# Optimization experiments

Measured on AMD Instinct MI355X. Metric: run time of the kernel, lower is better.

The kernel has to match this reference:

```python
import jax, jax.numpy as jnp
import numpy as np
import math

B, T, HID, H = 2, 2048, 2048, 16
D = HID // H  # 128
START_RATIO, RECENT_RATIO = 0.1, 0.25
ROPE_THETA = 10000.0


def setup_inputs() -> dict:
    key = jax.random.key(0)
    k1, k2, k3, k4, k5 = jax.random.split(key, 5)
    hidden_states = jax.random.normal(k1, (B, T, HID), jnp.float32)
    causal = jnp.tril(jnp.ones((T, T), bool))
    attention_mask = jnp.broadcast_to(
        jnp.where(causal, 0.0, jnp.finfo(jnp.float32).min)[None, None], (B, 1, T, T)
    )
    q_w = 0.02 * jax.random.normal(k2, (HID, HID), jnp.float32)
    k_w = 0.02 * jax.random.normal(k3, (HID, HID), jnp.float32)
    v_w = 0.02 * jax.random.normal(k4, (HID, HID), jnp.float32)
    o_w = 0.02 * jax.random.normal(k5, (HID, HID), jnp.float32)
    return dict(hidden_states=hidden_states, attention_mask=attention_mask,
                q_w=q_w, k_w=k_w, v_w=v_w, o_w=o_w)


def _rotate_half(x):
    x1, x2 = x[..., : D // 2], x[..., D // 2:]
    return jnp.concatenate([-x2, x1], axis=-1)


def _local_cam_mask(V, A_bar, recent_budget):
    # V: [B,H,K,D], A_bar: [B,H,K]
    K = V.shape[-2]
    m = recent_budget
    if m <= 0 or m >= K:
        return V
    evict_idx = max(0, min(K - m - 1, K - 1))
    ws = max(0, K - m)
    avg_window = jnp.clip(jnp.mean(A_bar[..., ws:], axis=-1), 1e-6, None)  # [B,H]
    prob = jnp.clip(A_bar[..., evict_idx] / avg_window, 0.0, 1.0)
    prob = jnp.nan_to_num(prob, nan=0.0, posinf=1.0, neginf=0.0)
    mask = jax.lax.stop_gradient(
        jax.random.bernoulli(jax.random.key(42), prob).astype(V.dtype)
    )  # [B,H]
    v_e = V[..., evict_idx, :] * mask[..., None] / m  # [B,H,D]
    return V.at[..., ws:, :].add(v_e[..., None, :])


def reference(hidden_states, attention_mask, q_w, k_w, v_w, o_w):
    MIN = jnp.finfo(hidden_states.dtype).min
    hs = jnp.nan_to_num(hidden_states, nan=0.0, posinf=1e4, neginf=-1e4)

    def proj(w):
        return (hs @ w.T).reshape(B, T, H, D).transpose(0, 2, 1, 3)  # [B,H,T,D]

    Q, K, V = proj(q_w), proj(k_w), proj(v_w)

    # rotary embedding (standard Llama)
    pos = jnp.arange(T, dtype=jnp.float32)
    inv_freq = 1.0 / (ROPE_THETA ** (jnp.arange(0, D, 2, dtype=jnp.float32) / D))
    freqs = pos[:, None] * inv_freq[None, :]  # [T, D/2]
    emb = jnp.concatenate([freqs, freqs], axis=-1)  # [T, D]
    cos, sin = jnp.cos(emb)[None, None], jnp.sin(emb)[None, None]
    Q = Q * cos + _rotate_half(Q) * sin
    K = K * cos + _rotate_half(K) * sin

    scores = jnp.einsum('bhtd,bhkd->bhtk', Q, K) / math.sqrt(D) + attention_mask
    scores = jnp.nan_to_num(scores, nan=MIN, posinf=MIN, neginf=MIN)
    attn = jax.nn.softmax(scores, axis=-1)  # [B,H,T,T]

    # first call: A_bar = detached last-row attention
    A_bar = jax.lax.stop_gradient(attn[..., -1, :])  # [B,H,T]

    k_len = T
    sb = max(0, min(int(START_RATIO * k_len), k_len))
    rb = max(0, min(int(RECENT_RATIO * k_len), k_len - sb))
    V = _local_cam_mask(V, A_bar, rb)

    attn_out = jnp.einsum('bhtk,bhkd->bhtd', attn, V)
    out = attn_out.transpose(0, 2, 1, 3).reshape(B, T, HID)
    return out @ o_w.T
```

## Files before the change

kernel.cpp:

```cpp
#include <hip/hip_runtime.h>
#include <cstdint>
#include <cstddef>


#define DEVINL __device__ __forceinline__

typedef float  f32x4  __attribute__((ext_vector_type(4)));
typedef __bf16 bf16x8 __attribute__((ext_vector_type(8)));

DEVINL float bf2f(unsigned short u){
  unsigned int x = ((unsigned int)u) << 16;
  return __builtin_bit_cast(float, x);
}
DEVINL void store_bf(unsigned short* p, float f){
  *(__bf16*)p = (__bf16)f;
}

DEVINL void load_lds16(const void* g, void* l){
  __builtin_amdgcn_global_load_lds(
      (const __attribute__((address_space(1))) void*)g,
      (__attribute__((address_space(3))) void*)l, 16, 0, 0);
}

#define QSCALE 0.127517432f

__global__ void cvt_all_kernel(const float* __restrict__ hs, const float* __restrict__ qw,
                               const float* __restrict__ kw, const float* __restrict__ vw,
                               const float* __restrict__ ow,
                               unsigned short* __restrict__ hsb, unsigned short* __restrict__ qwb,
                               unsigned short* __restrict__ kwb, unsigned short* __restrict__ vwb,
                               unsigned short* __restrict__ owb){
  int i = blockIdx.x * 256 + threadIdx.x;
  const float* s; unsigned short* d; int off;
  if (i < 2097152){ s = hs; d = hsb; off = i; }
  else {
    int j = i - 2097152; int w = j >> 20; off = j & 1048575;
    s = (w == 0) ? qw : (w == 1) ? kw : (w == 2) ? vw : ow;
    d = (w == 0) ? qwb : (w == 1) ? kwb : (w == 2) ? vwb : owb;
  }
  float4 v = reinterpret_cast<const float4*>(s)[off];
  unsigned short o[4];
  store_bf(&o[0], v.x); store_bf(&o[1], v.y); store_bf(&o[2], v.z); store_bf(&o[3], v.w);
  reinterpret_cast<uint2*>(d)[off] = *reinterpret_cast<uint2*>(o);
}

template<int MODE>
__global__ __launch_bounds__(256, 3)
void gemm_bt_kernel(const unsigned short* __restrict__ A,
                    const unsigned short* __restrict__ B,
                    unsigned short* __restrict__ Qo, unsigned short* __restrict__ Ko,
                    unsigned short* __restrict__ Vo, float* __restrict__ Co,
                    int M, int N, int K){
  __shared__ unsigned short As[128 * 64];
  __shared__ unsigned short Bs[128 * 64];
  const int tid = threadIdx.x, wave = tid >> 6, lane = tid & 63;
  const int m16 = lane & 15, quad = lane >> 4;
  const int m0 = blockIdx.y * 128, n0 = blockIdx.x * 128;
  const int wm = wave >> 1, wn = wave & 1;

  f32x4 acc[4][4] = {};

  for (int k0 = 0; k0 < K; k0 += 64){
    __syncthreads();
    #pragma unroll
    for (int i = 0; i < 4; ++i){
      int r  = wave * 32 + i * 8 + (lane >> 3);
      int c8 = (lane & 7) ^ (r & 7);
      load_lds16(A + (size_t)(m0 + r) * K + k0 + c8 * 8, &As[(wave * 32 + i * 8) * 64]);
      load_lds16(B + (size_t)(n0 + r) * K + k0 + c8 * 8, &Bs[(wave * 32 + i * 8) * 64]);
    }
    __syncthreads();
    #pragma unroll
    for (int kc = 0; kc < 2; ++kc){
      bf16x8 af[4], bfr[4];
      #pragma unroll
      for (int mt = 0; mt < 4; ++mt){
        int r = wm * 64 + mt * 16 + m16;
        af[mt] = *reinterpret_cast<const bf16x8*>(&As[(r * 8 + ((quad + 4 * kc) ^ (r & 7))) * 8]);
      }
      #pragma unroll
      for (int nt = 0; nt < 4; ++nt){
        int r = wn * 64 + nt * 16 + m16;
        bfr[nt] = *reinterpret_cast<const bf16x8*>(&Bs[(r * 8 + ((quad + 4 * kc) ^ (r & 7))) * 8]);
      }
      #pragma unroll
      for (int mt = 0; mt < 4; ++mt)
        #pragma unroll
        for (int nt = 0; nt < 4; ++nt)
          acc[mt][nt] = __builtin_amdgcn_mfma_f32_16x16x32_bf16(af[mt], bfr[nt], acc[mt][nt], 0, 0, 0);
    }
  }

  #pragma unroll
  for (int mt = 0; mt < 4; ++mt){
    #pragma unroll
    for (int nt = 0; nt < 4; ++nt){
      #pragma unroll
      for (int reg = 0; reg < 4; ++reg){
        int m = m0 + wm * 64 + mt * 16 + quad * 4 + reg;
        int n = n0 + wn * 64 + nt * 16 + m16;
        float v = acc[mt][nt][reg];
        if constexpr (MODE == 0){
          int which = n >> 11;
          int nn = n & 2047;
          int bq = m >> 11, t = m & 2047, hd = nn >> 7, dd = nn & 127;
          if (which == 0)
            store_bf(&Qo[((((size_t)bq) * 16 + hd) * 2048 + t) * 128 + dd], v);
          else if (which == 1)
            store_bf(&Ko[((((size_t)bq) * 16 + hd) * 2048 + t) * 128 + dd], v);
          else
            store_bf(&Vo[((((size_t)bq) * 16 + hd) * 128 + dd) * 2048 + t], v);
        } else {
          Co[(size_t)m * N + n] = v;
        }
      }
    }
  }
}

__global__ void rope_kernel(unsigned short* __restrict__ Q, unsigned short* __restrict__ K){
  int gid = blockIdx.x * 256 + threadIdx.x;
  int d2 = gid & 63;
  int t  = (gid >> 6) & 2047;
  int bh = (gid >> 17) & 31;
  int isK = gid >> 22;
  unsigned short* P = isK ? K : Q;
  float sc = isK ? 1.0f : QSCALE;
  size_t base = ((size_t)bh * 2048 + t) * 128;
  float x1 = bf2f(P[base + d2]);
  float x2 = bf2f(P[base + d2 + 64]);
  float inv = expf(-(float)d2 * 0.14391156606007266f);
  float fr = (float)t * inv;
  float sn, cs;
  sincosf(fr, &sn, &cs);
  store_bf(&P[base + d2],      (x1 * cs - x2 * sn) * sc);
  store_bf(&P[base + d2 + 64], (x2 * cs + x1 * sn) * sc);
}

DEVINL unsigned int rotl32(unsigned int x, int r){ return (x << r) | (x >> (32 - r)); }

__device__ float threefry_u01(int i){
  unsigned int c0 = (i < 16) ? (unsigned)i : (unsigned)(i - 16);
  unsigned int c1 = (i < 16) ? (unsigned)(i + 16) : (unsigned)i;
  bool hi = (i >= 16);
  unsigned int k0 = 0u, k1 = 42u, k2 = 0x1BD11BDAu ^ k0 ^ k1;
  unsigned int ks[3] = {k0, k1, k2};
  unsigned int x0 = c0 + k0, x1 = c1 + k1;
  const int R0[4] = {13, 15, 26, 6}, R1[4] = {17, 29, 16, 24};
  #pragma unroll
  for (int r = 0; r < 5; ++r){
    const int* RR = (r & 1) ? R1 : R0;
    #pragma unroll
    for (int j = 0; j < 4; ++j){ x0 += x1; x1 = rotl32(x1, RR[j]); x1 ^= x0; }
    x0 += ks[(r + 1) % 3];
    x1 += ks[(r + 2) % 3] + (unsigned)(r + 1);
  }
  unsigned int bits = hi ? x1 : x0;
  return __builtin_bit_cast(float, (bits >> 9) | 0x3f800000u) - 1.0f;
}

DEVINL float wred_max(float v){
  #pragma unroll
  for (int m = 1; m < 64; m <<= 1) v = fmaxf(v, __shfl_xor(v, m));
  return v;
}
DEVINL float wred_sum(float v){
  #pragma unroll
  for (int m = 1; m < 64; m <<= 1) v += __shfl_xor(v, m);
  return v;
}

__global__ __launch_bounds__(256)
void cam_kernel(const unsigned short* __restrict__ Q,
                const unsigned short* __restrict__ K,
                unsigned short* __restrict__ Vt){
  const int bh = blockIdx.x, tid = threadIdx.x;
  __shared__ float qv[128];
  __shared__ float redm[4], reds[4], redw[4];
  __shared__ float e1535s;
  __shared__ float bc0;
  if (tid < 128) qv[tid] = bf2f(Q[((size_t)bh * 2048 + 2047) * 128 + tid]);
  __syncthreads();

  float sc[8];
  float smax = -1e30f;
  #pragma unroll
  for (int j = 0; j < 8; ++j){
    int k = tid + j * 256;
    const uint4* kr4 = reinterpret_cast<const uint4*>(K + ((size_t)bh * 2048 + k) * 128);
    float acc = 0.f;
    #pragma unroll
    for (int c = 0; c < 16; ++c){
      uint4 pk = kr4[c];
      acc += qv[c * 8 + 0] * bf2f((unsigned short)(pk.x & 0xffff));
      acc += qv[c * 8 + 1] * bf2f((unsigned short)(pk.x >> 16));
      acc += qv[c * 8 + 2] * bf2f((unsigned short)(pk.y & 0xffff));
      acc += qv[c * 8 + 3] * bf2f((unsigned short)(pk.y >> 16));
      acc += qv[c * 8 + 4] * bf2f((unsigned short)(pk.z & 0xffff));
      acc += qv[c * 8 + 5] * bf2f((unsigned short)(pk.z >> 16));
      acc += qv[c * 8 + 6] * bf2f((unsigned short)(pk.w & 0xffff));
      acc += qv[c * 8 + 7] * bf2f((unsigned short)(pk.w >> 16));
    }
    sc[j] = acc;
    smax = fmaxf(smax, sc[j]);
  }
  int wave = tid >> 6, lane = tid & 63;
  float wm = wred_max(smax);
  if (lane == 0) redm[wave] = wm;
  __syncthreads();
  float M = fmaxf(fmaxf(redm[0], redm[1]), fmaxf(redm[2], redm[3]));
  float tsum = 0.f, wsum = 0.f;
  #pragma unroll
  for (int j = 0; j < 8; ++j){
    int k = tid + j * 256;
    float e = exp2f(sc[j] - M);
    if (k == 1535) e1535s = e;
    tsum += e;
    if (k >= 1536) wsum += e;
  }
  tsum = wred_sum(tsum); wsum = wred_sum(wsum);
  if (lane == 0){ reds[wave] = tsum; redw[wave] = wsum; }
  __syncthreads();
  if (tid == 0){
    float sum = reds[0] + reds[1] + reds[2] + reds[3];
    float wsm = redw[0] + redw[1] + redw[2] + redw[3];
    float abar = e1535s / sum;
    float avg  = fmaxf(wsm / (512.f * sum), 1e-6f);
    float pr   = abar / avg;
    pr = fminf(fmaxf(pr, 0.f), 1.f);
    float u = threefry_u01(bh);
    bc0 = (u < pr) ? (1.f / 512.f) : 0.f;
  }
  __syncthreads();
  float ves = bc0;
  if (ves != 0.f){
    for (int idx = tid; idx < 128 * 64; idx += 256){
      int d = idx >> 6, c = idx & 63;
      unsigned short* row = Vt + ((size_t)bh * 128 + d) * 2048;
      float ve = bf2f(row[1535]) * ves;
      uint4* p = reinterpret_cast<uint4*>(row + 1536) + c;
      uint4 pk = *p;
      unsigned short h[8];
      store_bf(&h[0], bf2f((unsigned short)(pk.x & 0xffff)) + ve);
      store_bf(&h[1], bf2f((unsigned short)(pk.x >> 16)) + ve);
      store_bf(&h[2], bf2f((unsigned short)(pk.y & 0xffff)) + ve);
      store_bf(&h[3], bf2f((unsigned short)(pk.y >> 16)) + ve);
      store_bf(&h[4], bf2f((unsigned short)(pk.z & 0xffff)) + ve);
      store_bf(&h[5], bf2f((unsigned short)(pk.z >> 16)) + ve);
      store_bf(&h[6], bf2f((unsigned short)(pk.w & 0xffff)) + ve);
      store_bf(&h[7], bf2f((unsigned short)(pk.w >> 16)) + ve);
      pk.x = (unsigned)h[0] | ((unsigned)h[1] << 16);
      pk.y = (unsigned)h[2] | ((unsigned)h[3] << 16);
      pk.z = (unsigned)h[4] | ((unsigned)h[5] << 16);
      pk.w = (unsigned)h[6] | ((unsigned)h[7] << 16);
      *p = pk;
    }
  }
}

__global__ __launch_bounds__(256, 2)
void flash_kernel(const unsigned short* __restrict__ Q,
                  const unsigned short* __restrict__ K,
                  const unsigned short* __restrict__ Vt,
                  unsigned short* __restrict__ AO){
  __shared__ unsigned short Qs[64 * 128];
  __shared__ unsigned short Ks[2][64 * 128];
  __shared__ unsigned short Vs[2][128 * 64];
  const int g = blockIdx.x, bh = blockIdx.y;
  const int tid = threadIdx.x, wave = tid >> 6, lane = tid & 63;
  const int m16 = lane & 15, quad = lane >> 4;
  unsigned short* Pw = Qs + wave * 2048;
  const int b = bh >> 4, h = bh & 15;

  bf16x8 onesf;
  #pragma unroll
  for (int j = 0; j < 8; ++j) onesf[j] = (__bf16)1.0f;

  #pragma unroll 1
  for (int phase = 0; phase < 2; ++phase){
    const int qt = phase ? (31 - g) : g;
    const int nk = qt + 1;

    {
      size_t qb = ((size_t)bh * 2048 + (size_t)qt * 64) * 128;
      #pragma unroll
      for (int i = 0; i < 4; ++i){
        int r   = wave * 16 + i * 4 + (lane >> 4);
        int c16 = (lane & 15) ^ (r & 15);
        load_lds16(Q + qb + (size_t)r * 128 + c16 * 8, &Qs[(wave * 16 + i * 4) * 128]);
      }
    }
    __syncthreads();
    bf16x8 qf[4];
    {
      int r = wave * 16 + m16;
      #pragma unroll
      for (int kc = 0; kc < 4; ++kc)
        qf[kc] = *reinterpret_cast<const bf16x8*>(&Qs[(r * 16 + ((quad + 4 * kc) ^ (r & 15))) * 8]);
    }

    f32x4 oacc[8] = {};
    f32x4 oaccL = {};
    f32x4 mst = {-1e30f, -1e30f, -1e30f, -1e30f};

    auto stageKV = [&](int kt, int buf){
      size_t kb = ((size_t)bh * 2048 + (size_t)kt * 64) * 128;
      #pragma unroll
      for (int i = 0; i < 4; ++i){
        int r   = wave * 16 + i * 4 + (lane >> 4);
        int c16 = (lane & 15) ^ (r & 15);
        load_lds16(K + kb + (size_t)r * 128 + c16 * 8, &Ks[buf][(wave * 16 + i * 4) * 128]);
      }
      size_t vb = (size_t)bh * 128 * 2048 + (size_t)kt * 64;
      #pragma unroll
      for (int i = 0; i < 4; ++i){
        int r  = wave * 32 + i * 8 + (lane >> 3);
        int c8 = (lane & 7) ^ (r & 7);
        load_lds16(Vt + vb + (size_t)r * 2048 + c8 * 8, &Vs[buf][(wave * 32 + i * 8) * 64]);
      }
    };

    stageKV(0, 0);
    #pragma unroll 1
    for (int t = 0; t < nk; ++t){
      const int buf = t & 1;
      __syncthreads();
      if (t + 1 < nk) stageKV(t + 1, buf ^ 1);

      f32x4 s[4] = {};
      #pragma unroll
      for (int kc = 0; kc < 4; ++kc){
        #pragma unroll
        for (int nt = 0; nt < 4; ++nt){
          int r = nt * 16 + m16;
          bf16x8 kf = *reinterpret_cast<const bf16x8*>(&Ks[buf][(r * 16 + ((quad + 4 * kc) ^ (r & 15))) * 8]);
          s[nt] = __builtin_amdgcn_mfma_f32_16x16x32_bf16(qf[kc], kf, s[nt], 0, 0, 0);
        }
      }
      if (t == nk - 1){
        int lrow = wave * 16 + quad * 4;
        #pragma unroll
        for (int nt = 0; nt < 4; ++nt)
          #pragma unroll
          for (int reg = 0; reg < 4; ++reg)
            if (nt * 16 + m16 > lrow + reg) s[nt][reg] = -1e30f;
      }
      f32x4 av;
      #pragma unroll
      for (int reg = 0; reg < 4; ++reg){
        float rm = fmaxf(fmaxf(s[0][reg], s[1][reg]), fmaxf(s[2][reg], s[3][reg]));
        rm = fmaxf(rm, __shfl_xor(rm, 1));
        rm = fmaxf(rm, __shfl_xor(rm, 2));
        rm = fmaxf(rm, __shfl_xor(rm, 4));
        rm = fmaxf(rm, __shfl_xor(rm, 8));
        float mold = mst[reg];
        float mnew = fmaxf(mold, rm);
        av[reg] = exp2f(mold - mnew);
        mst[reg] = mnew;
        #pragma unroll
        for (int nt = 0; nt < 4; ++nt)
          s[nt][reg] = exp2f(s[nt][reg] - mnew);
      }
      oaccL *= av;
      #pragma unroll
      for (int dt = 0; dt < 8; ++dt) oacc[dt] *= av;

      #pragma unroll
      for (int nt = 0; nt < 4; ++nt)
        #pragma unroll
        for (int reg = 0; reg < 4; ++reg){
          int r   = quad * 4 + reg;
          int col = nt * 16 + m16;
          store_bf(&Pw[(r * 8 + ((col >> 3) ^ (r & 7))) * 8 + (col & 7)], s[nt][reg]);
        }
      #pragma unroll
      for (int kc = 0; kc < 2; ++kc){
        bf16x8 pf = *reinterpret_cast<const bf16x8*>(&Pw[(m16 * 8 + ((quad + 4 * kc) ^ (m16 & 7))) * 8]);
        oaccL = __builtin_amdgcn_mfma_f32_16x16x32_bf16(pf, onesf, oaccL, 0, 0, 0);
        #pragma unroll
        for (int dt = 0; dt < 8; ++dt){
          int r = dt * 16 + m16;
          bf16x8 vf = *reinterpret_cast<const bf16x8*>(&Vs[buf][(r * 8 + ((quad + 4 * kc) ^ (r & 7))) * 8]);
          oacc[dt] = __builtin_amdgcn_mfma_f32_16x16x32_bf16(pf, vf, oacc[dt], 0, 0, 0);
        }
      }
    }

    #pragma unroll
    for (int reg = 0; reg < 4; ++reg){
      int tq = qt * 64 + wave * 16 + quad * 4 + reg;
      float inv = 1.0f / oaccL[reg];
      size_t ob = ((size_t)b * 2048 + tq) * 2048 + (size_t)h * 128;
      #pragma unroll
      for (int dt = 0; dt < 8; ++dt)
        store_bf(&AO[ob + dt * 16 + m16], oacc[dt][reg] * inv);
    }
  }
}

extern "C" void kernel_launch(void* const* d_in, const int* in_sizes, int n_in,
                              void* d_out, int out_size, void* d_ws, size_t ws_size,
                              hipStream_t stream){
  const float* hs = (const float*)d_in[0];
  const float* qw = (const float*)d_in[2];
  const float* kw = (const float*)d_in[3];
  const float* vw = (const float*)d_in[4];
  const float* ow = (const float*)d_in[5];

  char* ws = (char*)d_ws;
  const size_t MB = 1ull << 20;
  unsigned short* hsb = (unsigned short*)(ws);
  unsigned short* qwb = (unsigned short*)(ws + 16 * MB);
  unsigned short* kwb = (unsigned short*)(ws + 24 * MB);
  unsigned short* vwb = (unsigned short*)(ws + 32 * MB);
  unsigned short* owb = (unsigned short*)(ws + 40 * MB);
  unsigned short* Qb  = (unsigned short*)(ws + 48 * MB);
  unsigned short* Kb  = (unsigned short*)(ws + 64 * MB);
  unsigned short* Vtb = (unsigned short*)(ws + 80 * MB);
  unsigned short* AOb = (unsigned short*)(ws + 96 * MB);

  cvt_all_kernel<<<24576, 256, 0, stream>>>(hs, qw, kw, vw, ow, hsb, qwb, kwb, vwb, owb);

  gemm_bt_kernel<0><<<dim3(48, 32), 256, 0, stream>>>(hsb, qwb, Qb, Kb, Vtb, nullptr,
                                                      4096, 6144, 2048);

  rope_kernel<<<32768, 256, 0, stream>>>(Qb, Kb);
  cam_kernel<<<32, 256, 0, stream>>>(Qb, Kb, Vtb);
  flash_kernel<<<dim3(16, 32), 256, 0, stream>>>(Qb, Kb, Vtb, AOb);

  gemm_bt_kernel<2><<<dim3(16, 32), 256, 0, stream>>>(AOb, owb, nullptr, nullptr, nullptr,
                                                      (float*)d_out, 4096, 2048, 2048);
}
```

Baseline: 458.8 us.

## Double flash attention query tile to 128 rows for K/V reuse

```diff
diff --git a/kernel.cpp b/kernel.cpp
--- a/kernel.cpp
+++ b/kernel.cpp
@@ -263,138 +263,150 @@
                   const unsigned short* __restrict__ K,
                   const unsigned short* __restrict__ Vt,
                   unsigned short* __restrict__ AO){
-  __shared__ unsigned short Qs[64 * 128];
   __shared__ unsigned short Ks[2][64 * 128];
   __shared__ unsigned short Vs[2][128 * 64];
+  __shared__ unsigned short Ps[4 * 2048];
   const int g = blockIdx.x, bh = blockIdx.y;
   const int tid = threadIdx.x, wave = tid >> 6, lane = tid & 63;
   const int m16 = lane & 15, quad = lane >> 4;
-  unsigned short* Pw = Qs + wave * 2048;
+  unsigned short* Pw = Ps + wave * 2048;
   const int b = bh >> 4, h = bh & 15;
 
   bf16x8 onesf;
   #pragma unroll
   for (int j = 0; j < 8; ++j) onesf[j] = (__bf16)1.0f;
+
+  auto stageKV = [&](int kt, int buf){
+    size_t kb = ((size_t)bh * 2048 + (size_t)kt * 64) * 128;
+    #pragma unroll
+    for (int i = 0; i < 4; ++i){
+      int r   = wave * 16 + i * 4 + (lane >> 4);
+      int c16 = (lane & 15) ^ (r & 15);
+      load_lds16(K + kb + (size_t)r * 128 + c16 * 8, &Ks[buf][(wave * 16 + i * 4) * 128]);
+    }
+    size_t vb = (size_t)bh * 128 * 2048 + (size_t)kt * 64;
+    #pragma unroll
+    for (int i = 0; i < 4; ++i){
+      int r  = wave * 32 + i * 8 + (lane >> 3);
+      int c8 = (lane & 7) ^ (r & 7);
+      load_lds16(Vt + vb + (size_t)r * 2048 + c8 * 8, &Vs[buf][(wave * 32 + i * 8) * 64]);
+    }
+  };
 
   #pragma unroll 1
   for (int phase = 0; phase < 2; ++phase){
-    const int qt = phase ? (31 - g) : g;
-    const int nk = qt + 1;
-
-    {
-      size_t qb = ((size_t)bh * 2048 + (size_t)qt * 64) * 128;
-      #pragma unroll
-      for (int i = 0; i < 4; ++i){
-        int r   = wave * 16 + i * 4 + (lane >> 4);
-        int c16 = (lane & 15) ^ (r & 15);
-        load_lds16(Q + qb + (size_t)r * 128 + c16 * 8, &Qs[(wave * 16 + i * 4) * 128]);
-      }
-    }
-    __syncthreads();
-    bf16x8 qf[4];
-    {
-      int r = wave * 16 + m16;
+    const int qt = phase ? (15 - g) : g;
+    const int nk = 2 * qt + 2;
+
+    bf16x8 qf[2][4];
+    #pragma unroll
+    for (int mt = 0; mt < 2; ++mt){
+      size_t qrow = (size_t)bh * 2048 + (size_t)qt * 128 + wave * 32 + mt * 16 + m16;
       #pragma unroll
       for (int kc = 0; kc < 4; ++kc)
-        qf[kc] = *reinterpret_cast<const bf16x8*>(&Qs[(r * 16 + ((quad + 4 * kc) ^ (r & 15))) * 8]);
-    }
-
-    f32x4 oacc[8] = {};
-    f32x4 oaccL = {};
-    f32x4 mst = {-1e30f, -1e30f, -1e30f, -1e30f};
-
-    auto stageKV = [&](int kt, int buf){
-      size_t kb = ((size_t)bh * 2048 + (size_t)kt * 64) * 128;
-      #pragma unroll
-      for (int i = 0; i < 4; ++i){
-        int r   = wave * 16 + i * 4 + (lane >> 4);
-        int c16 = (lane & 15) ^ (r & 15);
-        load_lds16(K + kb + (size_t)r * 128 + c16 * 8, &Ks[buf][(wave * 16 + i * 4) * 128]);
-      }
-      size_t vb = (size_t)bh * 128 * 2048 + (size_t)kt * 64;
-      #pragma unroll
-      for (int i = 0; i < 4; ++i){
-        int r  = wave * 32 + i * 8 + (lane >> 3);
-        int c8 = (lane & 7) ^ (r & 7);
-        load_lds16(Vt + vb + (size_t)r * 2048 + c8 * 8, &Vs[buf][(wave * 32 + i * 8) * 64]);
-      }
-    };
-
-    stageKV(0, 0);
+        qf[mt][kc] = *reinterpret_cast<const bf16x8*>(Q + qrow * 128 + quad * 8 + kc * 32);
+    }
+
+    f32x4 oacc[2][8] = {};
+    f32x4 oaccL[2] = {};
+    f32x4 mst[2];
+    { f32x4 v = {-1e30f, -1e30f, -1e30f, -1e30f}; mst[0] = v; mst[1] = v; }
+
+    if (phase == 0) stageKV(0, 0);
+    else { __syncthreads(); stageKV(0, 0); }
+
     #pragma unroll 1
     for (int t = 0; t < nk; ++t){
       const int buf = t & 1;
       __syncthreads();
       if (t + 1 < nk) stageKV(t + 1, buf ^ 1);
 
-      f32x4 s[4] = {};
+      f32x4 s[2][4] = {};
       #pragma unroll
       for (int kc = 0; kc < 4; ++kc){
         #pragma unroll
         for (int nt = 0; nt < 4; ++nt){
           int r = nt * 16 + m16;
           bf16x8 kf = *reinterpret_cast<const bf16x8*>(&Ks[buf][(r * 16 + ((quad + 4 * kc) ^ (r & 15))) * 8]);
-          s[nt] = __builtin_amdgcn_mfma_f32_16x16x32_bf16(qf[kc], kf, s[nt], 0, 0, 0);
-        }
-      }
-      if (t == nk - 1){
-        int lrow = wave * 16 + quad * 4;
+          #pragma unroll
+          for (int mt = 0; mt < 2; ++mt)
+            s[mt][nt] = __builtin_amdgcn_mfma_f32_16x16x32_bf16(qf[mt][kc], kf, s[mt][nt], 0, 0, 0);
+        }
+      }
+      if (t >= 2 * qt){
+        #pragma unroll
+        for (int mt = 0; mt < 2; ++mt){
+          int lrow = qt * 128 + wave * 32 + mt * 16 + quad * 4;
+          int kbase = t * 64;
+          #pragma unroll
+          for (int nt = 0; nt < 4; ++nt)
+            #pragma unroll
+            for (int reg = 0; reg < 4; ++reg)
+              if (kbase + nt * 16 + m16 > lrow + reg) s[mt][nt][reg] = -1e30f;
+        }
+      }
+      #pragma unroll
+      for (int mt = 0; mt < 2; ++mt){
+        f32x4 av;
+        #pragma unroll
+        for (int reg = 0; reg < 4; ++reg){
+          float rm = fmaxf(fmaxf(s[mt][0][reg], s[mt][1][reg]),
+                           fmaxf(s[mt][2][reg], s[mt][3][reg]));
+          rm = fmaxf(rm, __shfl_xor(rm, 1));
+          rm = fmaxf(rm, __shfl_xor(rm, 2));
+          rm = fmaxf(rm, __shfl_xor(rm, 4));
+          rm = fmaxf(rm, __shfl_xor(rm, 8));
+          float mold = mst[mt][reg];
+          float mnew = fmaxf(mold, rm);
+          av[reg] = exp2f(mold - mnew);
+          mst[mt][reg] = mnew;
+          #pragma unroll
+          for (int nt = 0; nt < 4; ++nt)
+            s[mt][nt][reg] = exp2f(s[mt][nt][reg] - mnew);
+        }
+        oaccL[mt] *= av;
+        #pragma unroll
+        for (int dt = 0; dt < 8; ++dt) oacc[mt][dt] *= av;
         #pragma unroll
         for (int nt = 0; nt < 4; ++nt)
           #pragma unroll
-          for (int reg = 0; reg < 4; ++reg)
-            if (nt * 16 + m16 > lrow + reg) s[nt][reg] = -1e30f;
-      }
-      f32x4 av;
-      #pragma unroll
-      for (int reg = 0; reg < 4; ++reg){
-        float rm = fmaxf(fmaxf(s[0][reg], s[1][reg]), fmaxf(s[2][reg], s[3][reg]));
-        rm = fmaxf(rm, __shfl_xor(rm, 1));
-        rm = fmaxf(rm, __shfl_xor(rm, 2));
-        rm = fmaxf(rm, __shfl_xor(rm, 4));
-        rm = fmaxf(rm, __shfl_xor(rm, 8));
-        float mold = mst[reg];
-        float mnew = fmaxf(mold, rm);
-        av[reg] = exp2f(mold - mnew);
-        mst[reg] = mnew;
-        #pragma unroll
-        for (int nt = 0; nt < 4; ++nt)
-          s[nt][reg] = exp2f(s[nt][reg] - mnew);
-      }
-      oaccL *= av;
-      #pragma unroll
-      for (int dt = 0; dt < 8; ++dt) oacc[dt] *= av;
-
-      #pragma unroll
-      for (int nt = 0; nt < 4; ++nt)
-        #pragma unroll
-        for (int reg = 0; reg < 4; ++reg){
-          int r   = quad * 4 + reg;
-          int col = nt * 16 + m16;
-          store_bf(&Pw[(r * 8 + ((col >> 3) ^ (r & 7))) * 8 + (col & 7)], s[nt][reg]);
-        }
+          for (int reg = 0; reg < 4; ++reg){
+            int r   = mt * 16 + quad * 4 + reg;
+            int col = nt * 16 + m16;
+            store_bf(&Pw[(r * 8 + ((col >> 3) ^ (r & 7))) * 8 + (col & 7)], s[mt][nt][reg]);
+          }
+      }
       #pragma unroll
       for (int kc = 0; kc < 2; ++kc){
-        bf16x8 pf = *reinterpret_cast<const bf16x8*>(&Pw[(m16 * 8 + ((quad + 4 * kc) ^ (m16 & 7))) * 8]);
-        oaccL = __builtin_amdgcn_mfma_f32_16x16x32_bf16(pf, onesf, oaccL, 0, 0, 0);
+        bf16x8 pf[2];
+        #pragma unroll
+        for (int mt = 0; mt < 2; ++mt){
+          int rr = mt * 16 + m16;
+          pf[mt] = *reinterpret_cast<const bf16x8*>(&Pw[(rr * 8 + ((quad + 4 * kc) ^ (rr & 7))) * 8]);
+          oaccL[mt] = __builtin_amdgcn_mfma_f32_16x16x32_bf16(pf[mt], onesf, oaccL[mt], 0, 0, 0);
+        }
         #pragma unroll
         for (int dt = 0; dt < 8; ++dt){
           int r = dt * 16 + m16;
           bf16x8 vf = *reinterpret_cast<const bf16x8*>(&Vs[buf][(r * 8 + ((quad + 4 * kc) ^ (r & 7))) * 8]);
-          oacc[dt] = __builtin_amdgcn_mfma_f32_16x16x32_bf16(pf, vf, oacc[dt], 0, 0, 0);
-        }
-      }
-    }
-
-    #pragma unroll
-    for (int reg = 0; reg < 4; ++reg){
-      int tq = qt * 64 + wave * 16 + quad * 4 + reg;
-      float inv = 1.0f / oaccL[reg];
-      size_t ob = ((size_t)b * 2048 + tq) * 2048 + (size_t)h * 128;
-      #pragma unroll
-      for (int dt = 0; dt < 8; ++dt)
-        store_bf(&AO[ob + dt * 16 + m16], oacc[dt][reg] * inv);
-    }
+          #pragma unroll
+          for (int mt = 0; mt < 2; ++mt)
+            oacc[mt][dt] = __builtin_amdgcn_mfma_f32_16x16x32_bf16(pf[mt], vf, oacc[mt][dt], 0, 0, 0);
+        }
+      }
+    }
+
+    #pragma unroll
+    for (int mt = 0; mt < 2; ++mt)
+      #pragma unroll
+      for (int reg = 0; reg < 4; ++reg){
+        int tq = qt * 128 + wave * 32 + mt * 16 + quad * 4 + reg;
+        float inv = 1.0f / oaccL[mt][reg];
+        size_t ob = ((size_t)b * 2048 + tq) * 2048 + (size_t)h * 128;
+        #pragma unroll
+        for (int dt = 0; dt < 8; ++dt)
+          store_bf(&AO[ob + dt * 16 + m16], oacc[mt][dt][reg] * inv);
+      }
   }
 }
 
@@ -426,7 +438,7 @@
 
   rope_kernel<<<32768, 256, 0, stream>>>(Qb, Kb);
   cam_kernel<<<32, 256, 0, stream>>>(Qb, Kb, Vtb);
-  flash_kernel<<<dim3(16, 32), 256, 0, stream>>>(Qb, Kb, Vtb, AOb);
+  flash_kernel<<<dim3(8, 32), 256, 0, stream>>>(Qb, Kb, Vtb, AOb);
 
   gemm_bt_kernel<2><<<dim3(16, 32), 256, 0, stream>>>(AOb, owb, nullptr, nullptr, nullptr,
                                                       (float*)d_out, 4096, 2048, 2048);
```

Measured after the change: 484.3 us. +5.6%, slower.
